# Performance work log

Hardware: AMD Instinct MI355X
Metric: run time of the kernel (lower is better)

The kernel has to match this reference:

```python
import jax, jax.numpy as jnp
import numpy as np

N_USERS = 50000
N_ENT = 100000
N_INT = 5
EMB = 128
N_REL = 20
N_EDGES = 1000000
NNZ = 1000000
N_HOPS = 2
C_IDX = jnp.array([0, 1, 2, 3])
V_IDX = jnp.array([4, 5, 6, 7])
K_IDX = jnp.array([8, 9, 10, 11])
O_IDX = jnp.array([12, 13, 14, 15, 16, 17, 18, 19])


def setup_inputs() -> dict:
    key = jax.random.key(0)
    ks = jax.random.split(key, 9)
    return {
        "user_emb": jax.random.normal(ks[0], (N_USERS, EMB), jnp.float32) * 0.1,
        "entity_emb": jax.random.normal(ks[1], (N_ENT, EMB), jnp.float32) * 0.1,
        "intent_emb": jax.random.normal(ks[2], (N_INT, EMB), jnp.float32) * 0.1,
        "edge_index": jax.random.randint(ks[3], (2, N_EDGES), 0, N_ENT),
        "edge_type": jax.random.randint(ks[4], (N_EDGES,), 1, N_REL + 1),
        "interact_rows": jax.random.randint(ks[5], (NNZ,), 0, N_USERS),
        "interact_cols": jax.random.randint(ks[6], (NNZ,), 0, N_ENT),
        "interact_vals": jax.random.uniform(ks[7], (NNZ,), jnp.float32),
        "r_emb": jax.random.normal(ks[8], (N_REL, EMB), jnp.float32) * 0.1,
    }


def _scatter_mean(src, idx, n):
    s = jax.ops.segment_sum(src, idx, num_segments=n)
    c = jax.ops.segment_sum(jnp.ones((src.shape[0],), src.dtype), idx, num_segments=n)
    return jnp.where(c[:, None] > 0, s / jnp.maximum(c, 1.0)[:, None], 0.0)


def _intent_agg(vec, emb):
    # softmax over rows of (vec * emb).sum(-1), then attention-weighted mean
    att = jax.nn.softmax(jnp.sum(vec * emb, axis=1))
    return jnp.mean(att[:, None] * emb, axis=0)


def _l2norm(x):
    n = jnp.linalg.norm(x, axis=1, keepdims=True)
    return x / jnp.maximum(n, 1e-12)


def _dist_cor(t1, t2):
    d = t1.shape[0]
    t1 = t1[:, None]
    t2 = t2[:, None]
    a_ = 2.0 * (t1 @ t1.T)
    b_ = 2.0 * (t2 @ t2.T)
    t1s = t1 ** 2
    t2s = t2 ** 2
    a = jnp.sqrt(jnp.maximum(t1s - a_ + t1s.T, 0.0) + 1e-8)
    b = jnp.sqrt(jnp.maximum(t2s - b_ + t2s.T, 0.0) + 1e-8)
    A = a - a.mean(axis=0, keepdims=True) - a.mean(axis=1, keepdims=True) + a.mean()
    B = b - b.mean(axis=0, keepdims=True) - b.mean(axis=1, keepdims=True) + b.mean()
    d2 = float(d * d)
    dcov_AB = jnp.sqrt(jnp.maximum((A * B).sum() / d2, 0.0) + 1e-8)
    dcov_AA = jnp.sqrt(jnp.maximum((A * A).sum() / d2, 0.0) + 1e-8)
    dcov_BB = jnp.sqrt(jnp.maximum((B * B).sum() / d2, 0.0) + 1e-8)
    return dcov_AB / jnp.sqrt(dcov_AA * dcov_BB + 1e-8)


def _cul_cor(intent_emb):
    cor = 0.0
    for i in range(N_INT):
        for j in range(i + 1, N_INT):
            cor = cor + _dist_cor(intent_emb[i], intent_emb[j])
    return cor


def _forward(user_emb, entity_emb, intent_emb, edge_index, edge_type,
             interact_rows, interact_cols, interact_vals, r_emb):
    head, tail = edge_index[0], edge_index[1]
    cor = _cul_cor(intent_emb)
    res_e, res_u = entity_emb, user_emb
    e, u = entity_emb, user_emb
    for _ in range(N_HOPS):
        # edge gather-multiply-scatter_mean: [E,D]
        msg = e[tail] * r_emb[edge_type - 1]
        e_agg = _scatter_mean(msg, head, N_ENT)
        # intent attention over relation subsets
        all_intent = jnp.stack([
            _intent_agg(intent_emb[0], r_emb),
            _intent_agg(intent_emb[1], r_emb[C_IDX]),
            _intent_agg(intent_emb[2], r_emb[V_IDX]),
            _intent_agg(intent_emb[3], r_emb[K_IDX]),
            _intent_agg(intent_emb[4], r_emb[O_IDX]),
        ], axis=0)
        intent2 = (all_intent + intent_emb) / 2.0  # [5,D]
        # user-intent attention
        score = jax.nn.softmax(u @ intent2.T, axis=1)  # [U,5]
        # sparse.mm(interact_mat, entity_emb)
        u_agg = jax.ops.segment_sum(interact_vals[:, None] * e[interact_cols],
                                    interact_rows, num_segments=N_USERS)
        u_agg = u_agg * (score @ intent2) + u_agg
        e = _l2norm(e_agg)
        u = _l2norm(u_agg)
        res_e = res_e + e
        res_u = res_u + u
    return res_e, res_u, cor


def reference(user_emb, entity_emb, intent_emb, edge_index, edge_type,
              interact_rows, interact_cols, interact_vals, r_emb):
    return _forward(user_emb, entity_emb, intent_emb, edge_index, edge_type,
                    interact_rows, interact_cols, interact_vals, r_emb)
```

## Files before the change

### kernel.cpp

```cpp
#include <hip/hip_runtime.h>
#include <hip/hip_fp16.h>
#include <math.h>

#define N_USERS 50000
#define N_ENT   100000
#define N_INT   5
#define EMB     128
#define N_REL   20
#define N_EDGES 1000000
#define NNZ     1000000
#define SLOT    64
#define NPART   8
#define STAGE_CAP 131072
#define CSTRIDE 32
#define SITEMS  4
#define NCHUNK_S 256
#define EBLOCKS (N_ENT/8)
#define UBLOCKS (N_USERS/8)

union F4H8 { float4 f4; __half2 h2[4]; };

__global__ __launch_bounds__(256) void cor_pair_kernel(const float* __restrict__ intent,
                                                       float* __restrict__ partial) {
    __shared__ float t1[EMB], t2[EMB], rma[EMB], rmb[EMB];
    __shared__ float red[256];
    __shared__ float sh_mean_a, sh_mean_b;
    const int tid = threadIdx.x;
    const int p = blockIdx.x;
    const int pi[10] = {0,0,0,0,1,1,1,2,2,3};
    const int pj[10] = {1,2,3,4,2,3,4,3,4,4};

    if (tid < EMB) {
        t1[tid] = intent[pi[p]*EMB + tid];
        t2[tid] = intent[pj[p]*EMB + tid];
    }
    __syncthreads();
    if (tid < EMB) {
        float x1 = t1[tid], x2 = t2[tid];
        float sa = 0.f, sb = 0.f;
        for (int k = 0; k < EMB; ++k) {
            float da = x1 - t1[k];
            float db = x2 - t2[k];
            sa += sqrtf(da*da + 1e-8f);
            sb += sqrtf(db*db + 1e-8f);
        }
        rma[tid] = sa / (float)EMB;
        rmb[tid] = sb / (float)EMB;
    }
    __syncthreads();
    red[tid] = (tid < EMB) ? rma[tid] : 0.f;
    __syncthreads();
    for (int s = 128; s > 0; s >>= 1) { if (tid < s) red[tid] += red[tid+s]; __syncthreads(); }
    if (tid == 0) sh_mean_a = red[0] / (float)EMB;
    __syncthreads();
    red[tid] = (tid < EMB) ? rmb[tid] : 0.f;
    __syncthreads();
    for (int s = 128; s > 0; s >>= 1) { if (tid < s) red[tid] += red[tid+s]; __syncthreads(); }
    if (tid == 0) sh_mean_b = red[0] / (float)EMB;
    __syncthreads();
    const float mean_a = sh_mean_a, mean_b = sh_mean_b;

    float lab = 0.f, laa = 0.f, lbb = 0.f;
    for (int idx = tid; idx < EMB*EMB; idx += 256) {
        int r = idx >> 7, c = idx & (EMB-1);
        float da = t1[r] - t1[c];
        float db = t2[r] - t2[c];
        float av = sqrtf(da*da + 1e-8f);
        float bv = sqrtf(db*db + 1e-8f);
        float A = av - rma[r] - rma[c] + mean_a;
        float B = bv - rmb[r] - rmb[c] + mean_b;
        lab += A*B; laa += A*A; lbb += B*B;
    }
    red[tid] = lab; __syncthreads();
    for (int s = 128; s > 0; s >>= 1) { if (tid < s) red[tid] += red[tid+s]; __syncthreads(); }
    float sab = red[0]; __syncthreads();
    red[tid] = laa; __syncthreads();
    for (int s = 128; s > 0; s >>= 1) { if (tid < s) red[tid] += red[tid+s]; __syncthreads(); }
    float saa = red[0]; __syncthreads();
    red[tid] = lbb; __syncthreads();
    for (int s = 128; s > 0; s >>= 1) { if (tid < s) red[tid] += red[tid+s]; __syncthreads(); }
    float sbb = red[0]; __syncthreads();

    if (tid == 0) {
        const float d2 = (float)(EMB*EMB);
        float dab = sqrtf(fmaxf(sab/d2, 0.f) + 1e-8f);
        float daa = sqrtf(fmaxf(saa/d2, 0.f) + 1e-8f);
        float dbb = sqrtf(fmaxf(sbb/d2, 0.f) + 1e-8f);
        partial[p] = dab / sqrtf(daa*dbb + 1e-8f);
    }
}

__global__ void cor_sum_kernel(const float* __restrict__ partial, float* __restrict__ out_cor) {
    if (threadIdx.x == 0) {
        float s = 0.f;
        for (int i = 0; i < 10; ++i) s += partial[i];
        out_cor[0] = s;
    }
}

__global__ __launch_bounds__(128) void intent2_kernel(const float* __restrict__ intent,
                                                      const float* __restrict__ r_emb,
                                                      float* __restrict__ intent2) {
    const int i = blockIdx.x;
    const int d = threadIdx.x;
    __shared__ float red[EMB];
    __shared__ float dot[N_REL];
    int start, n;
    if      (i == 0) { start = 0;  n = 20; }
    else if (i == 1) { start = 0;  n = 4;  }
    else if (i == 2) { start = 4;  n = 4;  }
    else if (i == 3) { start = 8;  n = 4;  }
    else             { start = 12; n = 8;  }

    const float v = intent[i*EMB + d];
    for (int j = 0; j < n; ++j) {
        red[d] = v * r_emb[(start+j)*EMB + d];
        __syncthreads();
        for (int s = 64; s > 0; s >>= 1) { if (d < s) red[d] += red[d+s]; __syncthreads(); }
        if (d == 0) dot[j] = red[0];
        __syncthreads();
    }
    float m = -1e30f;
    for (int j = 0; j < n; ++j) m = fmaxf(m, dot[j]);
    float s = 0.f;
    float att[N_REL];
    for (int j = 0; j < n; ++j) { att[j] = expf(dot[j] - m); s += att[j]; }
    float out = 0.f;
    for (int j = 0; j < n; ++j) out += (att[j]/s) * r_emb[(start+j)*EMB + d];
    out /= (float)n;
    intent2[i*EMB + d] = 0.5f * (out + v);
}

__global__ __launch_bounds__(256) void conv_kernel(const float2* __restrict__ in,
                                                   __half2* __restrict__ out, int n) {
    int i = blockIdx.x*256 + threadIdx.x;
    if (i < n) { float2 v = in[i]; out[i] = __floats2half2_rn(v.x, v.y); }
}

__global__ __launch_bounds__(256) void stage_kernel(const int* __restrict__ head,
                                                    const int* __restrict__ tail,
                                                    const int* __restrict__ etype,
                                                    const int* __restrict__ irows,
                                                    const int* __restrict__ icols,
                                                    const float* __restrict__ ivals,
                                                    int* __restrict__ cursor,
                                                    uint2* __restrict__ stage_e,
                                                    uint2* __restrict__ stage_u) {
    __shared__ int l_cnt[2*NPART];
    __shared__ int l_base[2*NPART];
    const int TOTAL = N_EDGES + NNZ;
    const int tid = threadIdx.x;
    const int base = blockIdx.x * (256*SITEMS);

    if (tid < 2*NPART) l_cnt[tid] = 0;
    __syncthreads();

    int part[SITEMS], loc[SITEMS];
    unsigned w0[SITEMS], w1[SITEMS];
    bool act[SITEMS];
    #pragma unroll
    for (int t = 0; t < SITEMS; ++t) {
        const int i = base + t*256 + tid;
        act[t] = i < TOTAL;
        if (act[t]) {
            if (i < N_EDGES) {
                int h = head[i];
                part[t] = h / (N_ENT/NPART);
                w0[t] = (unsigned)h;
                w1[t] = (unsigned)(tail[i] | ((etype[i]-1) << 20));
            } else {
                int j = i - N_EDGES;
                int r = irows[j];
                part[t] = NPART + r / (N_USERS/NPART);
                unsigned q = (unsigned)(ivals[j]*32767.0f + 0.5f);
                w0[t] = (unsigned)r;
                w1[t] = (q << 17) | (unsigned)icols[j];
            }
            loc[t] = atomicAdd(&l_cnt[part[t]], 1);
        }
    }
    __syncthreads();
    if (tid < 2*NPART && l_cnt[tid] > 0)
        l_base[tid] = atomicAdd(&cursor[tid*CSTRIDE], l_cnt[tid]);
    __syncthreads();
    #pragma unroll
    for (int t = 0; t < SITEMS; ++t) {
        if (act[t]) {
            int pos = l_base[part[t]] + loc[t];
            if (pos < STAGE_CAP) {
                if (part[t] < NPART)
                    stage_e[(size_t)part[t]*STAGE_CAP + pos] = make_uint2(w0[t], w1[t]);
                else
                    stage_u[(size_t)(part[t]-NPART)*STAGE_CAP + pos] = make_uint2(w0[t], w1[t]);
            }
        }
    }
}

__global__ __launch_bounds__(256) void scatter_e_kernel(const uint2* __restrict__ stage_e,
                                                        const int* __restrict__ cursor,
                                                        int* __restrict__ cnt_e,
                                                        int* __restrict__ sorted_e) {
    const int part  = blockIdx.x & (NPART-1);
    const int chunk = blockIdx.x >> 3;
    const int n_e = min(cursor[part*CSTRIDE], STAGE_CAP);
    const uint2* se = stage_e + (size_t)part*STAGE_CAP;
    const int i0 = (chunk*256 + threadIdx.x) * 2;
    if (i0 >= n_e) return;
    uint4 v = *(const uint4*)(se + i0);
    int pos0 = atomicAdd(&cnt_e[v.x], 1);
    if (i0 + 1 < n_e) {
        int pos1 = atomicAdd(&cnt_e[v.z], 1);
        if (pos1 < SLOT) sorted_e[(size_t)v.z*SLOT + pos1] = (int)v.w;
    }
    if (pos0 < SLOT) sorted_e[(size_t)v.x*SLOT + pos0] = (int)v.y;
}

__global__ __launch_bounds__(256) void scatter_u_kernel(const uint2* __restrict__ stage_u,
                                                        const int* __restrict__ cursor,
                                                        int* __restrict__ cnt_u,
                                                        unsigned* __restrict__ sorted_u) {
    const int part  = blockIdx.x & (NPART-1);
    const int chunk = blockIdx.x >> 3;
    const int n_u = min(cursor[(NPART+part)*CSTRIDE], STAGE_CAP);
    const uint2* su = stage_u + (size_t)part*STAGE_CAP;
    const int i0 = (chunk*256 + threadIdx.x) * 2;
    if (i0 >= n_u) return;
    uint4 v = *(const uint4*)(su + i0);
    int pos0 = atomicAdd(&cnt_u[v.x], 1);
    if (i0 + 1 < n_u) {
        int pos1 = atomicAdd(&cnt_u[v.z], 1);
        if (pos1 < SLOT) sorted_u[(size_t)v.z*SLOT + pos1] = v.w;
    }
    if (pos0 < SLOT) sorted_u[(size_t)v.x*SLOT + pos0] = v.y;
}

__global__ __launch_bounds__(256) void gather_eu_kernel(const __half2* __restrict__ e_tab,
                                                        const int* __restrict__ cnt_e,
                                                        const int* __restrict__ sorted_e,
                                                        const float* __restrict__ r_emb,
                                                        const float2* __restrict__ base_e,
                                                        float2* __restrict__ res_e,
                                                        __half2* __restrict__ e_out,
                                                        const int* __restrict__ cnt_u,
                                                        const unsigned* __restrict__ sorted_u,
                                                        const float2* __restrict__ u_prev,
                                                        const float* __restrict__ i2,
                                                        const float2* __restrict__ base_u,
                                                        float2* __restrict__ res_u,
                                                        float2* __restrict__ u_out,
                                                        int store, int write_res) {
    __shared__ float2 s_i2[N_INT*64];
    __shared__ float  tr[4][2][132];

    const int wv   = threadIdx.x >> 6;
    const int lane = threadIdx.x & 63;
    const int g = lane >> 4, sl = lane & 15;
    const float4* e4 = (const float4*)e_tab;

    if (blockIdx.x < EBLOCKS) {
        const int row0 = blockIdx.x*8 + wv*2;
        const int row1 = row0 + 1;
        const int deg0 = min(cnt_e[row0], SLOT);
        const int deg1 = min(cnt_e[row1], SLOT);
        int p0 = (lane < deg0) ? sorted_e[(size_t)row0*SLOT + lane] : 0;
        int p1 = (lane < deg1) ? sorted_e[(size_t)row1*SLOT + lane] : 0;

        const float4* r4 = (const float4*)r_emb;
        float accA[8] = {0,0,0,0,0,0,0,0};
        float accB[8] = {0,0,0,0,0,0,0,0};

#define EFMA(ACC, RAW, PM) do { \
            F4H8 u_; u_.f4 = (RAW); \
            const __half* h_ = (const __half*)u_.h2; \
            const int rr_ = (PM) >> 20; \
            float4 w0_ = r4[rr_*32 + sl*2]; \
            float4 w1_ = r4[rr_*32 + sl*2 + 1]; \
            ACC[0] += __half2float(h_[0]) * w0_.x; \
            ACC[1] += __half2float(h_[1]) * w0_.y; \
            ACC[2] += __half2float(h_[2]) * w0_.z; \
            ACC[3] += __half2float(h_[3]) * w0_.w; \
            ACC[4] += __half2float(h_[4]) * w1_.x; \
            ACC[5] += __half2float(h_[5]) * w1_.y; \
            ACC[6] += __half2float(h_[6]) * w1_.z; \
            ACC[7] += __half2float(h_[7]) * w1_.w; \
        } while (0)

        const int dm = max(deg0, deg1);
        for (int k = 0; k < dm; k += 8) {
            const int meA = k + g, meB = k + 4 + g;
            const int pm00 = __shfl(p0, meA), pm01 = __shfl(p0, meB);
            const int pm10 = __shfl(p1, meA), pm11 = __shfl(p1, meB);
            const bool a00 = meA < deg0, a01 = meB < deg0;
            const bool a10 = meA < deg1, a11 = meB < deg1;
            float4 r00, r01, r10, r11;
            if (a00) r00 = e4[(size_t)(pm00 & 0xFFFFF)*16 + sl];
            if (a01) r01 = e4[(size_t)(pm01 & 0xFFFFF)*16 + sl];
            if (a10) r10 = e4[(size_t)(pm10 & 0xFFFFF)*16 + sl];
            if (a11) r11 = e4[(size_t)(pm11 & 0xFFFFF)*16 + sl];
            if (a00) EFMA(accA, r00, pm00);
            if (a01) EFMA(accA, r01, pm01);
            if (a10) EFMA(accB, r10, pm10);
            if (a11) EFMA(accB, r11, pm11);
        }
#undef EFMA

        #pragma unroll
        for (int j = 0; j < 8; ++j) {
            accA[j] += __shfl_xor(accA[j], 16);
            accA[j] += __shfl_xor(accA[j], 32);
            accB[j] += __shfl_xor(accB[j], 16);
            accB[j] += __shfl_xor(accB[j], 32);
        }
        const float invA = (deg0 > 0) ? 1.0f/(float)deg0 : 0.0f;
        const float invB = (deg1 > 0) ? 1.0f/(float)deg1 : 0.0f;
        float ssA = 0.f, ssB = 0.f;
        #pragma unroll
        for (int j = 0; j < 8; ++j) {
            accA[j] *= invA; ssA += accA[j]*accA[j];
            accB[j] *= invB; ssB += accB[j]*accB[j];
        }
        #pragma unroll
        for (int o = 8; o > 0; o >>= 1) {
            ssA += __shfl_xor(ssA, o);
            ssB += __shfl_xor(ssB, o);
        }
        const float invnA = 1.0f / fmaxf(sqrtf(ssA), 1e-12f);
        const float invnB = 1.0f / fmaxf(sqrtf(ssB), 1e-12f);
        #pragma unroll
        for (int j = 0; j < 8; ++j) { accA[j] *= invnA; accB[j] *= invnB; }

#define EPI(ROW, ACC) do { \
            size_t r16 = (size_t)(ROW)*16 + sl; \
            if (store) { \
                F4H8 u_; \
                u_.h2[0] = __floats2half2_rn(ACC[0], ACC[1]); \
                u_.h2[1] = __floats2half2_rn(ACC[2], ACC[3]); \
                u_.h2[2] = __floats2half2_rn(ACC[4], ACC[5]); \
                u_.h2[3] = __floats2half2_rn(ACC[6], ACC[7]); \
                ((float4*)e_out)[r16] = u_.f4; \
            } \
            if (write_res) { \
                F4H8 pv; pv.f4 = ((const float4*)e_tab)[r16]; \
                const float4* b4 = (const float4*)base_e; \
                float4 ba = b4[(size_t)(ROW)*32 + sl*2]; \
                float4 bb = b4[(size_t)(ROW)*32 + sl*2 + 1]; \
                float2 q0 = __half22float2(pv.h2[0]); \
                float2 q1 = __half22float2(pv.h2[1]); \
                float2 q2 = __half22float2(pv.h2[2]); \
                float2 q3 = __half22float2(pv.h2[3]); \
                float4 ra = make_float4(ba.x + q0.x + ACC[0], ba.y + q0.y + ACC[1], \
                                        ba.z + q1.x + ACC[2], ba.w + q1.y + ACC[3]); \
                float4 rb = make_float4(bb.x + q2.x + ACC[4], bb.y + q2.y + ACC[5], \
                                        bb.z + q3.x + ACC[6], bb.w + q3.y + ACC[7]); \
                ((float4*)res_e)[(size_t)(ROW)*32 + sl*2]     = ra; \
                ((float4*)res_e)[(size_t)(ROW)*32 + sl*2 + 1] = rb; \
            } \
        } while (0)

        if (g == 0)      EPI(row0, accA);
        else if (g == 1) EPI(row1, accB);
#undef EPI
    } else {
        for (int k = threadIdx.x; k < N_INT*64; k += 256) s_i2[k] = ((const float2*)i2)[k];
        __syncthreads();
        const int ub = blockIdx.x - EBLOCKS;
        const int row0 = ub*8 + wv*2;
        const int row1 = row0 + 1;
        const int deg0 = min(cnt_u[row0], SLOT);
        const int deg1 = min(cnt_u[row1], SLOT);
        unsigned p0 = (lane < deg0) ? sorted_u[(size_t)row0*SLOT + lane] : 0u;
        unsigned p1 = (lane < deg1) ? sorted_u[(size_t)row1*SLOT + lane] : 0u;

        const float qs = 1.0f/32767.0f;
        float accA[8] = {0,0,0,0,0,0,0,0};
        float accB[8] = {0,0,0,0,0,0,0,0};

#define UFMA(ACC, RAW, Q) do { \
            F4H8 u_; u_.f4 = (RAW); \
            const __half* h_ = (const __half*)u_.h2; \
            const float v_ = (float)((Q) >> 17) * qs; \
            ACC[0] += v_ * __half2float(h_[0]); \
            ACC[1] += v_ * __half2float(h_[1]); \
            ACC[2] += v_ * __half2float(h_[2]); \
            ACC[3] += v_ * __half2float(h_[3]); \
            ACC[4] += v_ * __half2float(h_[4]); \
            ACC[5] += v_ * __half2float(h_[5]); \
            ACC[6] += v_ * __half2float(h_[6]); \
            ACC[7] += v_ * __half2float(h_[7]); \
        } while (0)

        const int dm = max(deg0, deg1);
        for (int k = 0; k < dm; k += 8) {
            const int meA = k + g, meB = k + 4 + g;
            const unsigned q00 = __shfl(p0, meA), q01 = __shfl(p0, meB);
            const unsigned q10 = __shfl(p1, meA), q11 = __shfl(p1, meB);
            const bool a00 = meA < deg0, a01 = meB < deg0;
            const bool a10 = meA < deg1, a11 = meB < deg1;
            float4 r00, r01, r10, r11;
            if (a00) r00 = e4[(size_t)(q00 & 0x1FFFFu)*16 + sl];
            if (a01) r01 = e4[(size_t)(q01 & 0x1FFFFu)*16 + sl];
            if (a10) r10 = e4[(size_t)(q10 & 0x1FFFFu)*16 + sl];
            if (a11) r11 = e4[(size_t)(q11 & 0x1FFFFu)*16 + sl];
            if (a00) UFMA(accA, r00, q00);
            if (a01) UFMA(accA, r01, q01);
            if (a10) UFMA(accB, r10, q10);
            if (a11) UFMA(accB, r11, q11);
        }
#undef UFMA

        #pragma unroll
        for (int j = 0; j < 8; ++j) {
            accA[j] += __shfl_xor(accA[j], 16);
            accA[j] += __shfl_xor(accA[j], 32);
            accB[j] += __shfl_xor(accB[j], 16);
            accB[j] += __shfl_xor(accB[j], 32);
        }
        if (g == 0) {
            #pragma unroll
            for (int j = 0; j < 8; ++j) tr[wv][0][sl*8 + j] = accA[j];
        } else if (g == 1) {
            #pragma unroll
            for (int j = 0; j < 8; ++j) tr[wv][1][sl*8 + j] = accB[j];
        }
        __syncthreads();
        const float s00 = tr[wv][0][2*lane], s01 = tr[wv][0][2*lane + 1];
        const float s10 = tr[wv][1][2*lane], s11 = tr[wv][1][2*lane + 1];

        const size_t o0 = (size_t)row0*64 + lane;
        const size_t o1 = (size_t)row1*64 + lane;
        const float2 up0 = u_prev[o0];
        const float2 up1 = u_prev[o1];
        float dot0[N_INT], dot1[N_INT];
        #pragma unroll
        for (int i = 0; i < N_INT; ++i) {
            float2 w = s_i2[i*64 + lane];
            float pr0 = up0.x*w.x + up0.y*w.y;
            float pr1 = up1.x*w.x + up1.y*w.y;
            #pragma unroll
            for (int o = 32; o > 0; o >>= 1) {
                pr0 += __shfl_xor(pr0, o);
                pr1 += __shfl_xor(pr1, o);
            }
            dot0[i] = pr0; dot1[i] = pr1;
        }
        float m0 = dot0[0], m1 = dot1[0];
        #pragma unroll
        for (int i = 1; i < N_INT; ++i) { m0 = fmaxf(m0, dot0[i]); m1 = fmaxf(m1, dot1[i]); }
        float sm0 = 0.f, sm1 = 0.f;
        #pragma unroll
        for (int i = 0; i < N_INT; ++i) {
            dot0[i] = expf(dot0[i] - m0); sm0 += dot0[i];
            dot1[i] = expf(dot1[i] - m1); sm1 += dot1[i];
        }
        float f00 = 0.f, f01 = 0.f, f10 = 0.f, f11 = 0.f;
        #pragma unroll
        for (int i = 0; i < N_INT; ++i) {
            float a0 = dot0[i] / sm0;
            float a1 = dot1[i] / sm1;
            float2 w = s_i2[i*64 + lane];
            f00 += a0*w.x; f01 += a0*w.y;
            f10 += a1*w.x; f11 += a1*w.y;
        }
        float x00 = s00 * (1.0f + f00), x01 = s01 * (1.0f + f01);
        float x10 = s10 * (1.0f + f10), x11 = s11 * (1.0f + f11);
        float ss0 = x00*x00 + x01*x01;
        float ss1 = x10*x10 + x11*x11;
        #pragma unroll
        for (int o = 32; o > 0; o >>= 1) {
            ss0 += __shfl_xor(ss0, o);
            ss1 += __shfl_xor(ss1, o);
        }
        const float invn0 = 1.0f / fmaxf(sqrtf(ss0), 1e-12f);
        const float invn1 = 1.0f / fmaxf(sqrtf(ss1), 1e-12f);
        x00 *= invn0; x01 *= invn0;
        x10 *= invn1; x11 *= invn1;
        if (store) {
            u_out[o0] = make_float2(x00, x01);
            u_out[o1] = make_float2(x10, x11);
        }
        if (write_res) {
            float2 b0 = base_u[o0];
            float2 b1 = base_u[o1];
            res_u[o0] = make_float2(b0.x + up0.x + x00, b0.y + up0.y + x01);
            res_u[o1] = make_float2(b1.x + up1.x + x10, b1.y + up1.y + x11);
        }
    }
}

extern "C" void kernel_launch(void* const* d_in, const int* in_sizes, int n_in,
                              void* d_out, int out_size, void* d_ws, size_t ws_size,
                              hipStream_t stream) {
    const float* user_emb   = (const float*)d_in[0];
    const float* entity_emb = (const float*)d_in[1];
    const float* intent_emb = (const float*)d_in[2];
    const int*   edge_index = (const int*)  d_in[3];
    const int*   edge_type  = (const int*)  d_in[4];
    const int*   irows      = (const int*)  d_in[5];
    const int*   icols      = (const int*)  d_in[6];
    const float* ivals      = (const float*)d_in[7];
    const float* r_emb      = (const float*)d_in[8];

    float* out     = (float*)d_out;
    float* res_e   = out;
    float* res_u   = out + (size_t)N_ENT*EMB;
    float* out_cor = out + (size_t)N_ENT*EMB + (size_t)N_USERS*EMB;

    const int* head = edge_index;
    const int* tail = edge_index + N_EDGES;

    char* ws = (char*)d_ws;
    __half2* entF16 = (__half2*)ws;  ws += (size_t)N_ENT*EMB*2;
    __half2* eA     = (__half2*)ws;  ws += (size_t)N_ENT*EMB*2;
    float2*  uA     = (float2*)ws;   ws += (size_t)N_USERS*EMB*4;
    int*     sorted_e = (int*)ws;    ws += (size_t)N_ENT*SLOT*4;
    unsigned* sorted_u = (unsigned*)ws; ws += (size_t)N_USERS*SLOT*4;
    int* cnt_e = (int*)ws;           ws += (size_t)N_ENT*4;
    int* cnt_u = (int*)ws;           ws += (size_t)N_USERS*4;
    float* i2  = (float*)ws;         ws += N_INT*EMB*4;
    float* ws_cor = (float*)ws;      ws += 16*4;
    int* cursor = (int*)ws;          ws += 2*NPART*CSTRIDE*4;

    uint2* stage_e = (uint2*)eA;
    uint2* stage_u = (uint2*)uA;

    hipMemsetAsync(cnt_e, 0, (size_t)N_ENT*4, stream);
    hipMemsetAsync(cnt_u, 0, (size_t)N_USERS*4, stream);
    hipMemsetAsync(cursor, 0, 2*NPART*CSTRIDE*4, stream);

    cor_pair_kernel<<<10, 256, 0, stream>>>(intent_emb, ws_cor);
    cor_sum_kernel<<<1, 64, 0, stream>>>(ws_cor, out_cor);
    intent2_kernel<<<N_INT, 128, 0, stream>>>(intent_emb, r_emb, i2);
    conv_kernel<<<(N_ENT*64 + 255)/256, 256, 0, stream>>>((const float2*)entity_emb, entF16, N_ENT*64);

    stage_kernel<<<2048, 256, 0, stream>>>(head, tail, edge_type,
                                           irows, icols, ivals,
                                           cursor, stage_e, stage_u);
    scatter_e_kernel<<<NPART*NCHUNK_S, 256, 0, stream>>>(stage_e, cursor, cnt_e, sorted_e);
    scatter_u_kernel<<<NPART*NCHUNK_S, 256, 0, stream>>>(stage_u, cursor, cnt_u, sorted_u);

    const float2* ent2 = (const float2*)entity_emb;
    const float2* usr2 = (const float2*)user_emb;

    gather_eu_kernel<<<EBLOCKS + UBLOCKS, 256, 0, stream>>>(
        entF16, cnt_e, sorted_e, r_emb, ent2, (float2*)res_e, eA,
        cnt_u, sorted_u, usr2, i2, usr2, (float2*)res_u, uA, 1, 0);

    gather_eu_kernel<<<EBLOCKS + UBLOCKS, 256, 0, stream>>>(
        eA, cnt_e, sorted_e, r_emb, ent2, (float2*)res_e, eA,
        cnt_u, sorted_u, (const float2*)uA, i2, usr2, (float2*)res_u, uA, 0, 1);
}
```

Baseline: 503.5 us.

## Merge scatter kernels and process four rows per wave in gather

Fuses the entity and user scatter kernels into one launch, with each thread handling four staged items instead of two. The gather kernel now processes four rows per wavefront instead of two, halving the block count and issuing eight independent row loads per iteration to raise memory-level parallelism. The trade-off is higher register pressure and extra shared-memory transposes and barriers in the user path, which may cut occupancy.

```diff
diff --git a/kernel.cpp b/kernel.cpp
--- a/kernel.cpp
+++ b/kernel.cpp
@@ -14,9 +14,9 @@
 #define STAGE_CAP 131072
 #define CSTRIDE 32
 #define SITEMS  4
-#define NCHUNK_S 256
-#define EBLOCKS (N_ENT/8)
-#define UBLOCKS (N_USERS/8)
+#define NCH     128
+#define EBLOCKS (N_ENT/16)
+#define UBLOCKS (N_USERS/16)
 
 union F4H8 { float4 f4; __half2 h2[4]; };
 
@@ -197,42 +197,42 @@
     }
 }
 
-__global__ __launch_bounds__(256) void scatter_e_kernel(const uint2* __restrict__ stage_e,
-                                                        const int* __restrict__ cursor,
-                                                        int* __restrict__ cnt_e,
-                                                        int* __restrict__ sorted_e) {
-    const int part  = blockIdx.x & (NPART-1);
-    const int chunk = blockIdx.x >> 3;
-    const int n_e = min(cursor[part*CSTRIDE], STAGE_CAP);
-    const uint2* se = stage_e + (size_t)part*STAGE_CAP;
-    const int i0 = (chunk*256 + threadIdx.x) * 2;
-    if (i0 >= n_e) return;
-    uint4 v = *(const uint4*)(se + i0);
-    int pos0 = atomicAdd(&cnt_e[v.x], 1);
-    if (i0 + 1 < n_e) {
-        int pos1 = atomicAdd(&cnt_e[v.z], 1);
-        if (pos1 < SLOT) sorted_e[(size_t)v.z*SLOT + pos1] = (int)v.w;
-    }
-    if (pos0 < SLOT) sorted_e[(size_t)v.x*SLOT + pos0] = (int)v.y;
-}
-
-__global__ __launch_bounds__(256) void scatter_u_kernel(const uint2* __restrict__ stage_u,
-                                                        const int* __restrict__ cursor,
-                                                        int* __restrict__ cnt_u,
-                                                        unsigned* __restrict__ sorted_u) {
-    const int part  = blockIdx.x & (NPART-1);
-    const int chunk = blockIdx.x >> 3;
-    const int n_u = min(cursor[(NPART+part)*CSTRIDE], STAGE_CAP);
-    const uint2* su = stage_u + (size_t)part*STAGE_CAP;
-    const int i0 = (chunk*256 + threadIdx.x) * 2;
-    if (i0 >= n_u) return;
-    uint4 v = *(const uint4*)(su + i0);
-    int pos0 = atomicAdd(&cnt_u[v.x], 1);
-    if (i0 + 1 < n_u) {
-        int pos1 = atomicAdd(&cnt_u[v.z], 1);
-        if (pos1 < SLOT) sorted_u[(size_t)v.z*SLOT + pos1] = v.w;
-    }
-    if (pos0 < SLOT) sorted_u[(size_t)v.x*SLOT + pos0] = v.y;
+__global__ __launch_bounds__(256) void scatter_kernel(const uint2* __restrict__ stage_e,
+                                                      const uint2* __restrict__ stage_u,
+                                                      const int* __restrict__ cursor,
+                                                      int* __restrict__ cnt_e,
+                                                      int* __restrict__ cnt_u,
+                                                      int* __restrict__ sorted_e,
+                                                      unsigned* __restrict__ sorted_u) {
+    const int part = blockIdx.x & (NPART-1);
+    const int cid  = blockIdx.x >> 3;
+    const bool isE = cid < NCH;
+    const int chunk = isE ? cid : cid - NCH;
+    const int n = min(cursor[(isE ? part : NPART + part)*CSTRIDE], STAGE_CAP);
+    const uint2* s = (isE ? stage_e : stage_u) + (size_t)part*STAGE_CAP;
+    int* cnt = isE ? cnt_e : cnt_u;
+
+    const int i0 = (chunk*256 + threadIdx.x) * 4;
+    if (i0 >= n) return;
+    const bool h1 = i0 + 1 < n, h2 = i0 + 2 < n, h3 = i0 + 3 < n;
+    uint4 a = *(const uint4*)(s + i0);
+    uint4 b;
+    if (h2) b = *(const uint4*)(s + i0 + 2);
+    int pos0 = atomicAdd(&cnt[a.x], 1);
+    int pos1 = h1 ? atomicAdd(&cnt[a.z], 1) : 0;
+    int pos2 = h2 ? atomicAdd(&cnt[b.x], 1) : 0;
+    int pos3 = h3 ? atomicAdd(&cnt[b.z], 1) : 0;
+    if (isE) {
+        if (pos0 < SLOT)       sorted_e[(size_t)a.x*SLOT + pos0] = (int)a.y;
+        if (h1 && pos1 < SLOT) sorted_e[(size_t)a.z*SLOT + pos1] = (int)a.w;
+        if (h2 && pos2 < SLOT) sorted_e[(size_t)b.x*SLOT + pos2] = (int)b.y;
+        if (h3 && pos3 < SLOT) sorted_e[(size_t)b.z*SLOT + pos3] = (int)b.w;
+    } else {
+        if (pos0 < SLOT)       sorted_u[(size_t)a.x*SLOT + pos0] = a.y;
+        if (h1 && pos1 < SLOT) sorted_u[(size_t)a.z*SLOT + pos1] = a.w;
+        if (h2 && pos2 < SLOT) sorted_u[(size_t)b.x*SLOT + pos2] = b.y;
+        if (h3 && pos3 < SLOT) sorted_u[(size_t)b.z*SLOT + pos3] = b.w;
+    }
 }
 
 __global__ __launch_bounds__(256) void gather_eu_kernel(const __half2* __restrict__ e_tab,
@@ -259,16 +259,22 @@
     const float4* e4 = (const float4*)e_tab;
 
     if (blockIdx.x < EBLOCKS) {
-        const int row0 = blockIdx.x*8 + wv*2;
-        const int row1 = row0 + 1;
+        const int row0 = blockIdx.x*16 + wv*4;
+        const int row1 = row0 + 1, row2 = row0 + 2, row3 = row0 + 3;
         const int deg0 = min(cnt_e[row0], SLOT);
         const int deg1 = min(cnt_e[row1], SLOT);
+        const int deg2 = min(cnt_e[row2], SLOT);
+        const int deg3 = min(cnt_e[row3], SLOT);
         int p0 = (lane < deg0) ? sorted_e[(size_t)row0*SLOT + lane] : 0;
         int p1 = (lane < deg1) ? sorted_e[(size_t)row1*SLOT + lane] : 0;
+        int p2 = (lane < deg2) ? sorted_e[(size_t)row2*SLOT + lane] : 0;
+        int p3 = (lane < deg3) ? sorted_e[(size_t)row3*SLOT + lane] : 0;
 
         const float4* r4 = (const float4*)r_emb;
         float accA[8] = {0,0,0,0,0,0,0,0};
         float accB[8] = {0,0,0,0,0,0,0,0};
+        float accC[8] = {0,0,0,0,0,0,0,0};
+        float accD[8] = {0,0,0,0,0,0,0,0};
 
 #define EFMA(ACC, RAW, PM) do { \
             F4H8 u_; u_.f4 = (RAW); \
@@ -286,49 +292,71 @@
             ACC[7] += __half2float(h_[7]) * w1_.w; \
         } while (0)
 
-        const int dm = max(deg0, deg1);
+        const int dm = max(max(deg0, deg1), max(deg2, deg3));
         for (int k = 0; k < dm; k += 8) {
             const int meA = k + g, meB = k + 4 + g;
             const int pm00 = __shfl(p0, meA), pm01 = __shfl(p0, meB);
             const int pm10 = __shfl(p1, meA), pm11 = __shfl(p1, meB);
+            const int pm20 = __shfl(p2, meA), pm21 = __shfl(p2, meB);
+            const int pm30 = __shfl(p3, meA), pm31 = __shfl(p3, meB);
             const bool a00 = meA < deg0, a01 = meB < deg0;
             const bool a10 = meA < deg1, a11 = meB < deg1;
-            float4 r00, r01, r10, r11;
+            const bool a20 = meA < deg2, a21 = meB < deg2;
+            const bool a30 = meA < deg3, a31 = meB < deg3;
+            float4 r00, r01, r10, r11, r20, r21, r30, r31;
             if (a00) r00 = e4[(size_t)(pm00 & 0xFFFFF)*16 + sl];
             if (a01) r01 = e4[(size_t)(pm01 & 0xFFFFF)*16 + sl];
             if (a10) r10 = e4[(size_t)(pm10 & 0xFFFFF)*16 + sl];
             if (a11) r11 = e4[(size_t)(pm11 & 0xFFFFF)*16 + sl];
+            if (a20) r20 = e4[(size_t)(pm20 & 0xFFFFF)*16 + sl];
+            if (a21) r21 = e4[(size_t)(pm21 & 0xFFFFF)*16 + sl];
+            if (a30) r30 = e4[(size_t)(pm30 & 0xFFFFF)*16 + sl];
+            if (a31) r31 = e4[(size_t)(pm31 & 0xFFFFF)*16 + sl];
             if (a00) EFMA(accA, r00, pm00);
             if (a01) EFMA(accA, r01, pm01);
             if (a10) EFMA(accB, r10, pm10);
             if (a11) EFMA(accB, r11, pm11);
+            if (a20) EFMA(accC, r20, pm20);
+            if (a21) EFMA(accC, r21, pm21);
+            if (a30) EFMA(accD, r30, pm30);
+            if (a31) EFMA(accD, r31, pm31);
         }
 #undef EFMA
 
         #pragma unroll
         for (int j = 0; j < 8; ++j) {
-            accA[j] += __shfl_xor(accA[j], 16);
-            accA[j] += __shfl_xor(accA[j], 32);
-            accB[j] += __shfl_xor(accB[j], 16);
-            accB[j] += __shfl_xor(accB[j], 32);
+            accA[j] += __shfl_xor(accA[j], 16); accA[j] += __shfl_xor(accA[j], 32);
+            accB[j] += __shfl_xor(accB[j], 16); accB[j] += __shfl_xor(accB[j], 32);
+            accC[j] += __shfl_xor(accC[j], 16); accC[j] += __shfl_xor(accC[j], 32);
+            accD[j] += __shfl_xor(accD[j], 16); accD[j] += __shfl_xor(accD[j], 32);
         }
         const float invA = (deg0 > 0) ? 1.0f/(float)deg0 : 0.0f;
         const float invB = (deg1 > 0) ? 1.0f/(float)deg1 : 0.0f;
-        float ssA = 0.f, ssB = 0.f;
+        const float invC = (deg2 > 0) ? 1.0f/(float)deg2 : 0.0f;
+        const float invD = (deg3 > 0) ? 1.0f/(float)deg3 : 0.0f;
+        float ssA = 0.f, ssB = 0.f, ssC = 0.f, ssD = 0.f;
         #pragma unroll
         for (int j = 0; j < 8; ++j) {
             accA[j] *= invA; ssA += accA[j]*accA[j];
             accB[j] *= invB; ssB += accB[j]*accB[j];
+            accC[j] *= invC; ssC += accC[j]*accC[j];
+            accD[j] *= invD; ssD += accD[j]*accD[j];
         }
         #pragma unroll
         for (int o = 8; o > 0; o >>= 1) {
             ssA += __shfl_xor(ssA, o);
             ssB += __shfl_xor(ssB, o);
+            ssC += __shfl_xor(ssC, o);
+            ssD += __shfl_xor(ssD, o);
         }
         const float invnA = 1.0f / fmaxf(sqrtf(ssA), 1e-12f);
         const float invnB = 1.0f / fmaxf(sqrtf(ssB), 1e-12f);
-        #pragma unroll
-        for (int j = 0; j < 8; ++j) { accA[j] *= invnA; accB[j] *= invnB; }
+        const float invnC = 1.0f / fmaxf(sqrtf(ssC), 1e-12f);
+        const float invnD = 1.0f / fmaxf(sqrtf(ssD), 1e-12f);
+        #pragma unroll
+        for (int j = 0; j < 8; ++j) {
+            accA[j] *= invnA; accB[j] *= invnB; accC[j] *= invnC; accD[j] *= invnD;
+        }
 
 #define EPI(ROW, ACC) do { \
             size_t r16 = (size_t)(ROW)*16 + sl; \
@@ -360,21 +388,29 @@
 
         if (g == 0)      EPI(row0, accA);
         else if (g == 1) EPI(row1, accB);
+        else if (g == 2) EPI(row2, accC);
+        else             EPI(row3, accD);
 #undef EPI
     } else {
         for (int k = threadIdx.x; k < N_INT*64; k += 256) s_i2[k] = ((const float2*)i2)[k];
         __syncthreads();
         const int ub = blockIdx.x - EBLOCKS;
-        const int row0 = ub*8 + wv*2;
-        const int row1 = row0 + 1;
+        const int row0 = ub*16 + wv*4;
+        const int row1 = row0 + 1, row2 = row0 + 2, row3 = row0 + 3;
         const int deg0 = min(cnt_u[row0], SLOT);
         const int deg1 = min(cnt_u[row1], SLOT);
+        const int deg2 = min(cnt_u[row2], SLOT);
+        const int deg3 = min(cnt_u[row3], SLOT);
         unsigned p0 = (lane < deg0) ? sorted_u[(size_t)row0*SLOT + lane] : 0u;
         unsigned p1 = (lane < deg1) ? sorted_u[(size_t)row1*SLOT + lane] : 0u;
+        unsigned p2 = (lane < deg2) ? sorted_u[(size_t)row2*SLOT + lane] : 0u;
+        unsigned p3 = (lane < deg3) ? sorted_u[(size_t)row3*SLOT + lane] : 0u;
 
         const float qs = 1.0f/32767.0f;
         float accA[8] = {0,0,0,0,0,0,0,0};
         float accB[8] = {0,0,0,0,0,0,0,0};
+        float accC[8] = {0,0,0,0,0,0,0,0};
+        float accD[8] = {0,0,0,0,0,0,0,0};
 
 #define UFMA(ACC, RAW, Q) do { \
             F4H8 u_; u_.f4 = (RAW); \
@@ -390,31 +426,43 @@
             ACC[7] += v_ * __half2float(h_[7]); \
         } while (0)
 
-        const int dm = max(deg0, deg1);
+        const int dm = max(max(deg0, deg1), max(deg2, deg3));
         for (int k = 0; k < dm; k += 8) {
             const int meA = k + g, meB = k + 4 + g;
             const unsigned q00 = __shfl(p0, meA), q01 = __shfl(p0, meB);
             const unsigned q10 = __shfl(p1, meA), q11 = __shfl(p1, meB);
+            const unsigned q20 = __shfl(p2, meA), q21 = __shfl(p2, meB);
+            const unsigned q30 = __shfl(p3, meA), q31 = __shfl(p3, meB);
             const bool a00 = meA < deg0, a01 = meB < deg0;
             const bool a10 = meA < deg1, a11 = meB < deg1;
-            float4 r00, r01, r10, r11;
+            const bool a20 = meA < deg2, a21 = meB < deg2;
+            const bool a30 = meA < deg3, a31 = meB < deg3;
+            float4 r00, r01, r10, r11, r20, r21, r30, r31;
             if (a00) r00 = e4[(size_t)(q00 & 0x1FFFFu)*16 + sl];
             if (a01) r01 = e4[(size_t)(q01 & 0x1FFFFu)*16 + sl];
             if (a10) r10 = e4[(size_t)(q10 & 0x1FFFFu)*16 + sl];
             if (a11) r11 = e4[(size_t)(q11 & 0x1FFFFu)*16 + sl];
+            if (a20) r20 = e4[(size_t)(q20 & 0x1FFFFu)*16 + sl];
+            if (a21) r21 = e4[(size_t)(q21 & 0x1FFFFu)*16 + sl];
+            if (a30) r30 = e4[(size_t)(q30 & 0x1FFFFu)*16 + sl];
+            if (a31) r31 = e4[(size_t)(q31 & 0x1FFFFu)*16 + sl];
             if (a00) UFMA(accA, r00, q00);
             if (a01) UFMA(accA, r01, q01);
             if (a10) UFMA(accB, r10, q10);
             if (a11) UFMA(accB, r11, q11);
+            if (a20) UFMA(accC, r20, q20);
+            if (a21) UFMA(accC, r21, q21);
+            if (a30) UFMA(accD, r30, q30);
+            if (a31) UFMA(accD, r31, q31);
         }
 #undef UFMA
 
         #pragma unroll
         for (int j = 0; j < 8; ++j) {
-            accA[j] += __shfl_xor(accA[j], 16);
-            accA[j] += __shfl_xor(accA[j], 32);
-            accB[j] += __shfl_xor(accB[j], 16);
-            accB[j] += __shfl_xor(accB[j], 32);
+            accA[j] += __shfl_xor(accA[j], 16); accA[j] += __shfl_xor(accA[j], 32);
+            accB[j] += __shfl_xor(accB[j], 16); accB[j] += __shfl_xor(accB[j], 32);
+            accC[j] += __shfl_xor(accC[j], 16); accC[j] += __shfl_xor(accC[j], 32);
+            accD[j] += __shfl_xor(accD[j], 16); accD[j] += __shfl_xor(accD[j], 32);
         }
         if (g == 0) {
             #pragma unroll
@@ -426,64 +474,109 @@
         __syncthreads();
         const float s00 = tr[wv][0][2*lane], s01 = tr[wv][0][2*lane + 1];
         const float s10 = tr[wv][1][2*lane], s11 = tr[wv][1][2*lane + 1];
+        __syncthreads();
+        if (g == 0) {
+            #pragma unroll
+            for (int j = 0; j < 8; ++j) tr[wv][0][sl*8 + j] = accC[j];
+        } else if (g == 1) {
+            #pragma unroll
+            for (int j = 0; j < 8; ++j) tr[wv][1][sl*8 + j] = accD[j];
+        }
+        __syncthreads();
+        const float s20 = tr[wv][0][2*lane], s21 = tr[wv][0][2*lane + 1];
+        const float s30 = tr[wv][1][2*lane], s31 = tr[wv][1][2*lane + 1];
 
         const size_t o0 = (size_t)row0*64 + lane;
         const size_t o1 = (size_t)row1*64 + lane;
+        const size_t o2 = (size_t)row2*64 + lane;
+        const size_t o3 = (size_t)row3*64 + lane;
         const float2 up0 = u_prev[o0];
         const float2 up1 = u_prev[o1];
-        float dot0[N_INT], dot1[N_INT];
+        const float2 up2 = u_prev[o2];
+        const float2 up3 = u_prev[o3];
+        float dot0[N_INT], dot1[N_INT], dot2[N_INT], dot3[N_INT];
         #pragma unroll
         for (int i = 0; i < N_INT; ++i) {
             float2 w = s_i2[i*64 + lane];
             float pr0 = up0.x*w.x + up0.y*w.y;
             float pr1 = up1.x*w.x + up1.y*w.y;
+            float pr2 = up2.x*w.x + up2.y*w.y;
+            float pr3 = up3.x*w.x + up3.y*w.y;
             #pragma unroll
             for (int o = 32; o > 0; o >>= 1) {
                 pr0 += __shfl_xor(pr0, o);
                 pr1 += __shfl_xor(pr1, o);
+                pr2 += __shfl_xor(pr2, o);
+                pr3 += __shfl_xor(pr3, o);
             }
-            dot0[i] = pr0; dot1[i] = pr1;
-        }
-        float m0 = dot0[0], m1 = dot1[0];
-        #pragma unroll
-        for (int i = 1; i < N_INT; ++i) { m0 = fmaxf(m0, dot0[i]); m1 = fmaxf(m1, dot1[i]); }
-        float sm0 = 0.f, sm1 = 0.f;
+            dot0[i] = pr0; dot1[i] = pr1; dot2[i] = pr2; dot3[i] = pr3;
+        }
+        float m0 = dot0[0], m1 = dot1[0], m2 = dot2[0], m3 = dot3[0];
+        #pragma unroll
+        for (int i = 1; i < N_INT; ++i) {
+            m0 = fmaxf(m0, dot0[i]); m1 = fmaxf(m1, dot1[i]);
+            m2 = fmaxf(m2, dot2[i]); m3 = fmaxf(m3, dot3[i]);
+        }
+        float sm0 = 0.f, sm1 = 0.f, sm2 = 0.f, sm3 = 0.f;
         #pragma unroll
         for (int i = 0; i < N_INT; ++i) {
             dot0[i] = expf(dot0[i] - m0); sm0 += dot0[i];
             dot1[i] = expf(dot1[i] - m1); sm1 += dot1[i];
+            dot2[i] = expf(dot2[i] - m2); sm2 += dot2[i];
+            dot3[i] = expf(dot3[i] - m3); sm3 += dot3[i];
         }
         float f00 = 0.f, f01 = 0.f, f10 = 0.f, f11 = 0.f;
+        float f20 = 0.f, f21 = 0.f, f30 = 0.f, f31 = 0.f;
         #pragma unroll
         for (int i = 0; i < N_INT; ++i) {
             float a0 = dot0[i] / sm0;
             float a1 = dot1[i] / sm1;
+            float a2 = dot2[i] / sm2;
+            float a3 = dot3[i] / sm3;
             float2 w = s_i2[i*64 + lane];
             f00 += a0*w.x; f01 += a0*w.y;
             f10 += a1*w.x; f11 += a1*w.y;
+            f20 += a2*w.x; f21 += a2*w.y;
+            f30 += a3*w.x; f31 += a3*w.y;
         }
         float x00 = s00 * (1.0f + f00), x01 = s01 * (1.0f + f01);
         float x10 = s10 * (1.0f + f10), x11 = s11 * (1.0f + f11);
+        float x20 = s20 * (1.0f + f20), x21 = s21 * (1.0f + f21);
+        float x30 = s30 * (1.0f + f30), x31 = s31 * (1.0f + f31);
         float ss0 = x00*x00 + x01*x01;
         float ss1 = x10*x10 + x11*x11;
+        float ss2 = x20*x20 + x21*x21;
+        float ss3 = x30*x30 + x31*x31;
         #pragma unroll
         for (int o = 32; o > 0; o >>= 1) {
             ss0 += __shfl_xor(ss0, o);
             ss1 += __shfl_xor(ss1, o);
+            ss2 += __shfl_xor(ss2, o);
+            ss3 += __shfl_xor(ss3, o);
         }
         const float invn0 = 1.0f / fmaxf(sqrtf(ss0), 1e-12f);
         const float invn1 = 1.0f / fmaxf(sqrtf(ss1), 1e-12f);
+        const float invn2 = 1.0f / fmaxf(sqrtf(ss2), 1e-12f);
+        const float invn3 = 1.0f / fmaxf(sqrtf(ss3), 1e-12f);
         x00 *= invn0; x01 *= invn0;
         x10 *= invn1; x11 *= invn1;
+        x20 *= invn2; x21 *= invn2;
+        x30 *= invn3; x31 *= invn3;
         if (store) {
             u_out[o0] = make_float2(x00, x01);
             u_out[o1] = make_float2(x10, x11);
+            u_out[o2] = make_float2(x20, x21);
+            u_out[o3] = make_float2(x30, x31);
         }
         if (write_res) {
             float2 b0 = base_u[o0];
             float2 b1 = base_u[o1];
+            float2 b2 = base_u[o2];
+            float2 b3 = base_u[o3];
             res_u[o0] = make_float2(b0.x + up0.x + x00, b0.y + up0.y + x01);
             res_u[o1] = make_float2(b1.x + up1.x + x10, b1.y + up1.y + x11);
+            res_u[o2] = make_float2(b2.x + up2.x + x20, b2.y + up2.y + x21);
+            res_u[o3] = make_float2(b3.x + up3.x + x30, b3.y + up3.y + x31);
         }
     }
 }
@@ -536,8 +629,8 @@
     stage_kernel<<<2048, 256, 0, stream>>>(head, tail, edge_type,
                                            irows, icols, ivals,
                                            cursor, stage_e, stage_u);
-    scatter_e_kernel<<<NPART*NCHUNK_S, 256, 0, stream>>>(stage_e, cursor, cnt_e, sorted_e);
-    scatter_u_kernel<<<NPART*NCHUNK_S, 256, 0, stream>>>(stage_u, cursor, cnt_u, sorted_u);
+    scatter_kernel<<<NPART*2*NCH, 256, 0, stream>>>(stage_e, stage_u, cursor,
+                                                    cnt_e, cnt_u, sorted_e, sorted_u);
 
     const float2* ent2 = (const float2*)entity_emb;
     const float2* usr2 = (const float2*)user_emb;
```

Measured after the change: 535.8 us. 6.4% more time.
